# Optimization experiments

Measured on AMD Instinct MI355X. Metric: run time of the kernel, lower is better.

The kernel has to match this reference:

```python
import jax, jax.numpy as jnp
import numpy as np

B, L_R, H = 8, 128, 512
CTX_LEN, STATE_NUM, ACT_NUM = 256, 32, 32
L_SRC = CTX_LEN + STATE_NUM + ACT_NUM
N_VOCAB = 32000
N_TOPIC = 4096


def setup_inputs() -> dict:
    key = jax.random.key(0)
    ks = jax.random.split(key, 9)
    return {
        "dec_out": jax.random.normal(ks[0], (B, L_R, H), jnp.float32),
        "src_hidden": jax.random.normal(ks[1], (B, L_SRC, H), jnp.float32),
        "W_gen": jax.random.normal(ks[2], (H, N_VOCAB), jnp.float32) * 0.02,
        "b_gen": jnp.zeros((N_VOCAB,), jnp.float32),
        "src_mask": jax.random.randint(ks[3], (B, 1, L_SRC), 0, 2, jnp.int32),
        "context": jax.random.randint(ks[4], (B, CTX_LEN), 0, N_VOCAB, jnp.int32),
        "tp": jax.random.randint(ks[5], (B, STATE_NUM), 0, N_TOPIC, jnp.int32),
        "action": jax.random.randint(ks[6], (B, ACT_NUM), 0, N_TOPIC, jnp.int32),
        "loc2glo": jax.random.randint(ks[7], (N_TOPIC,), 0, N_VOCAB, jnp.int32),
    }


def _scatter_vocab(prob, idx):
    # prob: [L_r, L_seg], idx: [L_seg] global-vocab ids -> [L_r, n_vocab]
    # duplicate indices accumulate, matching torch scatter_add / one-hot bmm
    return jnp.zeros((prob.shape[0], N_VOCAB), prob.dtype).at[:, idx].add(prob)


def reference(dec_out, src_hidden, W_gen, b_gen, src_mask, context, tp, action, loc2glo):
    # gen logits: [B, L_r, n_vocab]
    gen_logit = jnp.einsum("blh,hv->blv", dec_out, W_gen) + b_gen
    # copy logits over concatenated source: [B, L_r, L_src]
    copy_logit = jnp.einsum("blh,bsh->bls", dec_out, src_hidden)
    copy_logit = jnp.where(src_mask == 0, jnp.float32(-1e9), copy_logit)
    logits = jnp.concatenate([gen_logit, copy_logit], axis=-1)
    logits = logits * (H ** -0.5)  # op.scale_prj
    probs = jax.nn.softmax(logits, axis=-1)

    gen_prob = probs[:, :, :N_VOCAB]
    copy_ctx = probs[:, :, N_VOCAB:N_VOCAB + CTX_LEN]
    copy_tp = probs[:, :, N_VOCAB + CTX_LEN:N_VOCAB + CTX_LEN + STATE_NUM]
    copy_ar = probs[:, :, N_VOCAB + CTX_LEN + STATE_NUM:]

    scatter = jax.vmap(_scatter_vocab)
    ctx_prob = scatter(copy_ctx, context)                 # replaces one-hot bmm
    tp_prob = scatter(copy_tp, loc2glo[tp])               # scatter_add via loc2glo gather
    ar_prob = scatter(copy_ar, loc2glo[action])

    return gen_prob + ctx_prob + tp_prob + ar_prob
```

## Files before the change

kernel.cpp:

```cpp
#include <hip/hip_runtime.h>
#include <stdint.h>
#include <stddef.h>

#define NV    32000
#define HDIM  512
#define LSRC  320
#define MROWS 1024
#define SCALEF 0.044194173824159216f

typedef unsigned short u16;
typedef unsigned int   u32;
typedef __attribute__((ext_vector_type(8))) short short8;
typedef __attribute__((ext_vector_type(4))) float floatx4;

__device__ __forceinline__ u16 f2bf(float f) {
  u32 x = __float_as_uint(f);
  return (u16)((x + 0x7fffu + ((x >> 16) & 1u)) >> 16);
}

typedef __attribute__((address_space(1))) void gvoid;
typedef __attribute__((address_space(3))) void lvoid;
__device__ __forceinline__ void cp16(const u16* g, u16* l) {
  __builtin_amdgcn_global_load_lds((gvoid*)g, (lvoid*)l, 16, 0, 0);
}

__global__ __launch_bounds__(256) void k_conv(const float* __restrict__ dec,
                                              const float* __restrict__ srch,
                                              u16* __restrict__ Ab,
                                              u16* __restrict__ Sb,
                                              float* __restrict__ rowSum) {
  if (blockIdx.x < 256) {
    if (blockIdx.x == 0) {
      ((float4*)rowSum)[threadIdx.x] = (float4){0.f, 0.f, 0.f, 0.f};
    }
    int t = blockIdx.x * 256 + threadIdx.x;
    int o = t * 8;
    int ki = o & 31;
    int mi = (o >> 5) & 255;
    int kt = (o >> 13) & 15;
    int mt = o >> 17;
    const float* s = dec + (size_t)(mt * 256 + mi) * HDIM + kt * 32 + ki;
    float4 a = ((const float4*)s)[0];
    float4 b = ((const float4*)s)[1];
    union { u16 h[8]; uint4 v; } pk;
    pk.h[0] = f2bf(a.x); pk.h[1] = f2bf(a.y); pk.h[2] = f2bf(a.z); pk.h[3] = f2bf(a.w);
    pk.h[4] = f2bf(b.x); pk.h[5] = f2bf(b.y); pk.h[6] = f2bf(b.z); pk.h[7] = f2bf(b.w);
    *(uint4*)(Ab + o) = pk.v;
  } else {
    int t = (blockIdx.x - 256) * 256 + threadIdx.x;
    int o = t * 8;
    int ki = o & 31;
    int ni = (o >> 5) & 127;
    int kt = (o >> 12) & 15;
    int r  = o >> 16;
    int st = r % 3, b = r / 3;
    int s = st * 128 + ni;
    uint4 v;
    if (s < LSRC) {
      const float* p = srch + ((size_t)b * LSRC + s) * HDIM + kt * 32 + ki;
      float4 a = ((const float4*)p)[0];
      float4 c = ((const float4*)p)[1];
      union { u16 h[8]; uint4 u; } pk;
      pk.h[0] = f2bf(a.x); pk.h[1] = f2bf(a.y); pk.h[2] = f2bf(a.z); pk.h[3] = f2bf(a.w);
      pk.h[4] = f2bf(c.x); pk.h[5] = f2bf(c.y); pk.h[6] = f2bf(c.z); pk.h[7] = f2bf(c.w);
      v = pk.u;
    } else {
      v = (uint4){0u, 0u, 0u, 0u};
    }
    *(uint4*)(Sb + o) = v;
  }
}

__global__ __launch_bounds__(256) void k_convW(const float* __restrict__ W,
                                               u16* __restrict__ Wb) {
  __shared__ u16 lds[256 * 36];
  int tileId = blockIdx.x;
  int nt = tileId >> 4, kt = tileId & 15;
  int t = threadIdx.x;
  const float* src = W + (size_t)kt * 32 * NV + (size_t)nt * 256;
#pragma unroll
  for (int i = 0; i < 8; ++i) {
    int f = t + 256 * i;
    int kin = f >> 6, n4 = f & 63;
    float4 v = *(const float4*)(src + (size_t)kin * NV + n4 * 4);
    int base = (n4 * 4) * 36 + kin;
    lds[base]       = f2bf(v.x);
    lds[base + 36]  = f2bf(v.y);
    lds[base + 72]  = f2bf(v.z);
    lds[base + 108] = f2bf(v.w);
  }
  __syncthreads();
  u16* dst = Wb + (size_t)tileId * 8192;
#pragma unroll
  for (int j = 0; j < 4; ++j) {
    int o = t * 8 + j * 2048;
    int ni = o >> 5, ki0 = o & 31;
    const u16* p = &lds[ni * 36 + ki0];
    uint2 x = *(const uint2*)p;
    uint2 y = *(const uint2*)(p + 4);
    uint4 v; v.x = x.x; v.y = x.y; v.z = y.x; v.w = y.y;
    *(uint4*)(dst + o) = v;
  }
}

__global__ __launch_bounds__(512, 2) void k_gemm(const u16* __restrict__ Ab,
                                                 const u16* __restrict__ Wb,
                                                 const float* __restrict__ bgen,
                                                 u16* __restrict__ wsE,
                                                 float* __restrict__ rowSum) {
  __shared__ u16 As[3][8192];
  __shared__ u16 Bs[3][8192];
  int bid = blockIdx.x;
  int xcd = bid & 7, rem = bid >> 3;
  int wgid = (xcd < 4 ? xcd * 63 : 252 + (xcd - 4) * 62) + rem;
  int x = wgid & 3, y = wgid >> 2;
  int t = threadIdx.x;
  int wid = t >> 6, lane = t & 63;
  int wm = wid >> 2, wn = wid & 3;
  int quad = lane >> 4, l16 = lane & 15;

  const u16* At = Ab + (size_t)x * (16 * 8192);
  const u16* Bt = Wb + (size_t)y * (16 * 8192);
  const u16* Ag0 = At + wid * 512 + lane * 8;
  const u16* Bg0 = Bt + wid * 512 + lane * 8;

  floatx4 acc[8][4];
#pragma unroll
  for (int i = 0; i < 8; ++i)
#pragma unroll
    for (int j = 0; j < 4; ++j) acc[i][j] = (floatx4){0.f, 0.f, 0.f, 0.f};

#pragma unroll
  for (int p = 0; p < 2; ++p) {
    const u16* ag = Ag0 + p * 8192;
    const u16* bg = Bg0 + p * 8192;
    cp16(ag,        &As[p][wid * 512]);
    cp16(ag + 4096, &As[p][wid * 512 + 4096]);
    cp16(bg,        &Bs[p][wid * 512]);
    cp16(bg + 4096, &Bs[p][wid * 512 + 4096]);
  }

#pragma unroll
  for (int kt = 0; kt < 16; ++kt) {
    const int cb = kt % 3;
    asm volatile("s_waitcnt lgkmcnt(0)" ::: "memory");
    if (kt < 15) asm volatile("s_waitcnt vmcnt(4)" ::: "memory");
    else         asm volatile("s_waitcnt vmcnt(0)" ::: "memory");
    __builtin_amdgcn_s_barrier();
    asm volatile("" ::: "memory");
    if (kt < 14) {
      const int sb = (kt + 2) % 3;
      const u16* ag = Ag0 + (kt + 2) * 8192;
      const u16* bg = Bg0 + (kt + 2) * 8192;
      cp16(ag,        &As[sb][wid * 512]);
      cp16(ag + 4096, &As[sb][wid * 512 + 4096]);
      cp16(bg,        &Bs[sb][wid * 512]);
      cp16(bg + 4096, &Bs[sb][wid * 512 + 4096]);
    }
    short8 aR[8], bR[4];
#pragma unroll
    for (int mt = 0; mt < 8; ++mt)
      aR[mt] = *(const short8*)&As[cb][(wm * 128 + mt * 16 + l16) * 32 + quad * 8];
#pragma unroll
    for (int nt = 0; nt < 4; ++nt)
      bR[nt] = *(const short8*)&Bs[cb][(wn * 64 + nt * 16 + l16) * 32 + quad * 8];
    __builtin_amdgcn_s_setprio(1);
#pragma unroll
    for (int mt = 0; mt < 8; ++mt)
#pragma unroll
      for (int nt = 0; nt < 4; ++nt)
        acc[mt][nt] = __builtin_amdgcn_mfma_f32_16x16x32_bf16(bR[nt], aR[mt],
                                                              acc[mt][nt], 0, 0, 0);
    __builtin_amdgcn_s_setprio(0);
  }

  int row0 = x * 256 + wm * 128;
  int col0 = y * 256 + wn * 64;
  float bq[4][4];
#pragma unroll
  for (int nt = 0; nt < 4; ++nt) {
    float4 v = *(const float4*)(bgen + col0 + nt * 16 + quad * 4);
    bq[nt][0] = v.x * SCALEF; bq[nt][1] = v.y * SCALEF;
    bq[nt][2] = v.z * SCALEF; bq[nt][3] = v.w * SCALEF;
  }
#pragma unroll
  for (int mt = 0; mt < 8; ++mt) {
    int row = row0 + mt * 16 + l16;
    float rsum = 0.f;
#pragma unroll
    for (int nt = 0; nt < 4; ++nt) {
      float e0 = __expf(fmaf(acc[mt][nt][0], SCALEF, bq[nt][0]));
      float e1 = __expf(fmaf(acc[mt][nt][1], SCALEF, bq[nt][1]));
      float e2 = __expf(fmaf(acc[mt][nt][2], SCALEF, bq[nt][2]));
      float e3 = __expf(fmaf(acc[mt][nt][3], SCALEF, bq[nt][3]));
      uint2 pk;
      pk.x = (u32)f2bf(e0) | ((u32)f2bf(e1) << 16);
      pk.y = (u32)f2bf(e2) | ((u32)f2bf(e3) << 16);
      *(uint2*)(wsE + (size_t)row * NV + col0 + nt * 16 + quad * 4) = pk;
      rsum += (e0 + e1) + (e2 + e3);
    }
    rsum += __shfl_xor(rsum, 16, 64);
    rsum += __shfl_xor(rsum, 32, 64);
    if (lane < 16) atomicAdd(&rowSum[row], rsum);
  }
}

__global__ __launch_bounds__(256) void k_copy(const u16* __restrict__ Ab,
                                              const u16* __restrict__ Sb,
                                              const int* __restrict__ mask,
                                              float* __restrict__ wsCopy,
                                              float* __restrict__ rowSum) {
  __shared__ u16 As[3][4096];
  __shared__ u16 Bs[3][4096];
  int bid = blockIdx.x;
  int b = bid / 3, st = bid % 3;
  int t = threadIdx.x;
  int wid = t >> 6, lane = t & 63;
  int wm = wid >> 1, wn = wid & 1;
  int quad = lane >> 4, l16 = lane & 15;

  const u16* At = Ab + (size_t)(b >> 1) * (16 * 8192) + (b & 1) * 4096;
  const u16* Bt = Sb + (size_t)(b * 3 + st) * (16 * 4096);
  const u16* Ag0 = At + wid * 1024 + lane * 8;
  const u16* Bg0 = Bt + wid * 1024 + lane * 8;

  floatx4 acc[4][4];
#pragma unroll
  for (int i = 0; i < 4; ++i)
#pragma unroll
    for (int j = 0; j < 4; ++j) acc[i][j] = (floatx4){0.f, 0.f, 0.f, 0.f};

#pragma unroll
  for (int p = 0; p < 2; ++p) {
    const u16* ag = Ag0 + p * 8192;
    const u16* bg = Bg0 + p * 4096;
    cp16(ag,       &As[p][wid * 1024]);
    cp16(ag + 512, &As[p][wid * 1024 + 512]);
    cp16(bg,       &Bs[p][wid * 1024]);
    cp16(bg + 512, &Bs[p][wid * 1024 + 512]);
  }

#pragma unroll
  for (int kt = 0; kt < 16; ++kt) {
    const int cb = kt % 3;
    asm volatile("s_waitcnt lgkmcnt(0)" ::: "memory");
    if (kt < 15) asm volatile("s_waitcnt vmcnt(4)" ::: "memory");
    else         asm volatile("s_waitcnt vmcnt(0)" ::: "memory");
    __builtin_amdgcn_s_barrier();
    asm volatile("" ::: "memory");
    if (kt < 14) {
      const int sb = (kt + 2) % 3;
      const u16* ag = Ag0 + (kt + 2) * 8192;
      const u16* bg = Bg0 + (kt + 2) * 4096;
      cp16(ag,       &As[sb][wid * 1024]);
      cp16(ag + 512, &As[sb][wid * 1024 + 512]);
      cp16(bg,       &Bs[sb][wid * 1024]);
      cp16(bg + 512, &Bs[sb][wid * 1024 + 512]);
    }
    short8 aR[4], bR[4];
#pragma unroll
    for (int mt = 0; mt < 4; ++mt)
      aR[mt] = *(const short8*)&As[cb][(wm * 64 + mt * 16 + l16) * 32 + quad * 8];
#pragma unroll
    for (int nt = 0; nt < 4; ++nt)
      bR[nt] = *(const short8*)&Bs[cb][(wn * 64 + nt * 16 + l16) * 32 + quad * 8];
#pragma unroll
    for (int mt = 0; mt < 4; ++mt)
#pragma unroll
      for (int nt = 0; nt < 4; ++nt)
        acc[mt][nt] = __builtin_amdgcn_mfma_f32_16x16x32_bf16(bR[nt], aR[mt],
                                                              acc[mt][nt], 0, 0, 0);
  }

  int row0 = b * 128 + wm * 64;
  int sBase = st * 128 + wn * 64;
  if (sBase < LSRC) {
    int mq[4][4];
#pragma unroll
    for (int nt = 0; nt < 4; ++nt) {
      int4 v = *(const int4*)(mask + b * LSRC + sBase + nt * 16 + quad * 4);
      mq[nt][0] = v.x; mq[nt][1] = v.y; mq[nt][2] = v.z; mq[nt][3] = v.w;
    }
#pragma unroll
    for (int mt = 0; mt < 4; ++mt) {
      int row = row0 + mt * 16 + l16;
      float rsum = 0.f;
#pragma unroll
      for (int nt = 0; nt < 4; ++nt) {
        float4 ev;
        ev.x = mq[nt][0] ? __expf(acc[mt][nt][0] * SCALEF) : 0.f;
        ev.y = mq[nt][1] ? __expf(acc[mt][nt][1] * SCALEF) : 0.f;
        ev.z = mq[nt][2] ? __expf(acc[mt][nt][2] * SCALEF) : 0.f;
        ev.w = mq[nt][3] ? __expf(acc[mt][nt][3] * SCALEF) : 0.f;
        *(float4*)(wsCopy + (size_t)row * LSRC + sBase + nt * 16 + quad * 4) = ev;
        rsum += (ev.x + ev.y) + (ev.z + ev.w);
      }
      rsum += __shfl_xor(rsum, 16, 64);
      rsum += __shfl_xor(rsum, 32, 64);
      if (lane < 16) atomicAdd(&rowSum[row], rsum);
    }
  }
}

__global__ __launch_bounds__(512) void k_norm(const u16* __restrict__ wsE,
                                              const float* __restrict__ wsCopy,
                                              const float* __restrict__ rowSum,
                                              const int* __restrict__ context,
                                              const int* __restrict__ tp,
                                              const int* __restrict__ action,
                                              const int* __restrict__ loc2glo,
                                              float* __restrict__ out) {
  int r = blockIdx.x, b = r >> 7;
  float inv = 1.0f / rowSum[r];
  const uint2* src = (const uint2*)(wsE + (size_t)r * NV);
  float4* dst = (float4*)(out + (size_t)r * NV);
  for (int c = threadIdx.x; c < NV / 4; c += 512) {
    uint2 v = src[c];
    float4 o;
    o.x = __uint_as_float(v.x << 16) * inv;
    o.y = __uint_as_float(v.x & 0xffff0000u) * inv;
    o.z = __uint_as_float(v.y << 16) * inv;
    o.w = __uint_as_float(v.y & 0xffff0000u) * inv;
    dst[c] = o;
  }
  __syncthreads();
  int t = threadIdx.x;
  float* op = out + (size_t)r * NV;
  if (t < 256) {
    atomicAdd(op + context[b * 256 + t], wsCopy[r * LSRC + t] * inv);
  } else if (t < 288) {
    int i = t - 256;
    atomicAdd(op + loc2glo[tp[b * 32 + i]], wsCopy[r * LSRC + 256 + i] * inv);
  } else if (t < 320) {
    int i = t - 288;
    atomicAdd(op + loc2glo[action[b * 32 + i]], wsCopy[r * LSRC + 288 + i] * inv);
  }
}

extern "C" void kernel_launch(void* const* d_in, const int* in_sizes, int n_in,
                              void* d_out, int out_size, void* d_ws, size_t ws_size,
                              hipStream_t stream) {
  const float* dec  = (const float*)d_in[0];
  const float* srch = (const float*)d_in[1];
  const float* Wg   = (const float*)d_in[2];
  const float* bg   = (const float*)d_in[3];
  const int*   mask = (const int*)d_in[4];
  const int*   ctx  = (const int*)d_in[5];
  const int*   tp   = (const int*)d_in[6];
  const int*   act  = (const int*)d_in[7];
  const int*   l2g  = (const int*)d_in[8];
  float* out = (float*)d_out;

  char* ws = (char*)d_ws;
  u16*   Wb      = (u16*)(ws);
  u16*   wsE     = (u16*)(ws + 32768000);
  u16*   Ab      = (u16*)(ws + 98304000);
  float* wsCopy  = (float*)(ws + 99352576);
  float* rowSum  = (float*)(ws + 100663296);
  u16*   Sb      = (u16*)(ws + 100667392);

  hipLaunchKernelGGL(k_conv, dim3(1024), dim3(256), 0, stream, dec, srch, Ab, Sb, rowSum);
  hipLaunchKernelGGL(k_convW, dim3(2000), dim3(256), 0, stream, Wg, Wb);
  hipLaunchKernelGGL(k_gemm, dim3(500), dim3(512), 0, stream, Ab, Wb, bg, wsE, rowSum);
  hipLaunchKernelGGL(k_copy, dim3(24), dim3(256), 0, stream, Ab, Sb, mask, wsCopy, rowSum);
  hipLaunchKernelGGL(k_norm, dim3(MROWS), dim3(512), 0, stream, wsE, wsCopy, rowSum,
                     ctx, tp, act, l2g, out);
}
```

Before: 324.8 us.

## Fold copy-logit GEMM into main GEMM grid and deepen LDS pipeline

Removes the separate k_copy launch. The copy logits now run as 12 extra 256x256 tiles in the main GEMM grid (512 blocks, a clean 64 per XCD), with the source hidden states repacked into 256-wide tiles that pair two batches. The GEMM main loop goes from 3 to 4 LDS stages and splits each k-step into two half-MFMA phases with staggered async loads and extra barriers, aiming for better load/compute overlap. The copy tiles waste some compute on cross-batch products that are masked off, and the larger LDS footprint (128 KB per block) may limit occupancy.

```diff
diff --git a/kernel.cpp b/kernel.cpp
--- a/kernel.cpp
+++ b/kernel.cpp
@@ -23,6 +23,7 @@
 __device__ __forceinline__ void cp16(const u16* g, u16* l) {
   __builtin_amdgcn_global_load_lds((gvoid*)g, (lvoid*)l, 16, 0, 0);
 }
+#define BARRIER() do { __builtin_amdgcn_s_barrier(); asm volatile("" ::: "memory"); } while (0)
 
 __global__ __launch_bounds__(256) void k_conv(const float* __restrict__ dec,
                                               const float* __restrict__ srch,
@@ -50,19 +51,23 @@
     int t = (blockIdx.x - 256) * 256 + threadIdx.x;
     int o = t * 8;
     int ki = o & 31;
-    int ni = (o >> 5) & 127;
-    int kt = (o >> 12) & 15;
-    int r  = o >> 16;
-    int st = r % 3, b = r / 3;
-    int s = st * 128 + ni;
+    int ni = (o >> 5) & 255;
+    int kt = (o >> 13) & 15;
+    int r  = o >> 17;
+    int yt = r % 3, x = r / 3;
+    int c = yt * 256 + ni;
+    int b, s, valid;
+    if (c < 320)      { b = x * 2;     s = c;       valid = 1; }
+    else if (c < 640) { b = x * 2 + 1; s = c - 320; valid = 1; }
+    else              { b = 0; s = 0; valid = 0; }
     uint4 v;
-    if (s < LSRC) {
+    if (valid) {
       const float* p = srch + ((size_t)b * LSRC + s) * HDIM + kt * 32 + ki;
       float4 a = ((const float4*)p)[0];
-      float4 c = ((const float4*)p)[1];
+      float4 cc = ((const float4*)p)[1];
       union { u16 h[8]; uint4 u; } pk;
-      pk.h[0] = f2bf(a.x); pk.h[1] = f2bf(a.y); pk.h[2] = f2bf(a.z); pk.h[3] = f2bf(a.w);
-      pk.h[4] = f2bf(c.x); pk.h[5] = f2bf(c.y); pk.h[6] = f2bf(c.z); pk.h[7] = f2bf(c.w);
+      pk.h[0] = f2bf(a.x);  pk.h[1] = f2bf(a.y);  pk.h[2] = f2bf(a.z);  pk.h[3] = f2bf(a.w);
+      pk.h[4] = f2bf(cc.x); pk.h[5] = f2bf(cc.y); pk.h[6] = f2bf(cc.z); pk.h[7] = f2bf(cc.w);
       v = pk.u;
     } else {
       v = (uint4){0u, 0u, 0u, 0u};
@@ -105,14 +110,17 @@
 
 __global__ __launch_bounds__(512, 2) void k_gemm(const u16* __restrict__ Ab,
                                                  const u16* __restrict__ Wb,
+                                                 const u16* __restrict__ Sb,
                                                  const float* __restrict__ bgen,
+                                                 const int* __restrict__ mask,
                                                  u16* __restrict__ wsE,
+                                                 float* __restrict__ wsCopy,
                                                  float* __restrict__ rowSum) {
-  __shared__ u16 As[3][8192];
-  __shared__ u16 Bs[3][8192];
+  __shared__ u16 As[4][8192];
+  __shared__ u16 Bs[4][8192];
   int bid = blockIdx.x;
-  int xcd = bid & 7, rem = bid >> 3;
-  int wgid = (xcd < 4 ? xcd * 63 : 252 + (xcd - 4) * 62) + rem;
+  int xcd = bid & 7;
+  int wgid = xcd * 64 + (bid >> 3);
   int x = wgid & 3, y = wgid >> 2;
   int t = threadIdx.x;
   int wid = t >> 6, lane = t & 63;
@@ -120,7 +128,8 @@
   int quad = lane >> 4, l16 = lane & 15;
 
   const u16* At = Ab + (size_t)x * (16 * 8192);
-  const u16* Bt = Wb + (size_t)y * (16 * 8192);
+  const u16* Bt = (y < 125) ? (Wb + (size_t)y * (16 * 8192))
+                            : (Sb + (size_t)(x * 3 + (y - 125)) * (16 * 8192));
   const u16* Ag0 = At + wid * 512 + lane * 8;
   const u16* Bg0 = Bt + wid * 512 + lane * 8;
 
@@ -131,7 +140,7 @@
     for (int j = 0; j < 4; ++j) acc[i][j] = (floatx4){0.f, 0.f, 0.f, 0.f};
 
 #pragma unroll
-  for (int p = 0; p < 2; ++p) {
+  for (int p = 0; p < 3; ++p) {
     const u16* ag = Ag0 + p * 8192;
     const u16* bg = Bg0 + p * 8192;
     cp16(ag,        &As[p][wid * 512]);
@@ -139,150 +148,108 @@
     cp16(bg,        &Bs[p][wid * 512]);
     cp16(bg + 4096, &Bs[p][wid * 512 + 4096]);
   }
-
-#pragma unroll
-  for (int kt = 0; kt < 16; ++kt) {
-    const int cb = kt % 3;
+  asm volatile("s_waitcnt vmcnt(8)" ::: "memory");
+  BARRIER();
+
+#pragma unroll
+  for (int h = 0; h < 16; ++h) {
+    const int slot = h & 3;
+    const int ps = (h + 3) & 3;
+    const u16* ag = Ag0 + (h + 3) * 8192;
+    const u16* bg = Bg0 + (h + 3) * 8192;
+    short8 aR[4], bR[4];
+#pragma unroll
+    for (int mt = 0; mt < 4; ++mt)
+      aR[mt] = *(const short8*)&As[slot][(wm * 128 + mt * 16 + l16) * 32 + quad * 8];
+#pragma unroll
+    for (int nt = 0; nt < 4; ++nt)
+      bR[nt] = *(const short8*)&Bs[slot][(wn * 64 + nt * 16 + l16) * 32 + quad * 8];
+    if (h < 13) {
+      cp16(ag, &As[ps][wid * 512]);
+      cp16(bg, &Bs[ps][wid * 512]);
+    }
+    BARRIER();
     asm volatile("s_waitcnt lgkmcnt(0)" ::: "memory");
-    if (kt < 15) asm volatile("s_waitcnt vmcnt(4)" ::: "memory");
-    else         asm volatile("s_waitcnt vmcnt(0)" ::: "memory");
-    __builtin_amdgcn_s_barrier();
-    asm volatile("" ::: "memory");
-    if (kt < 14) {
-      const int sb = (kt + 2) % 3;
-      const u16* ag = Ag0 + (kt + 2) * 8192;
-      const u16* bg = Bg0 + (kt + 2) * 8192;
-      cp16(ag,        &As[sb][wid * 512]);
-      cp16(ag + 4096, &As[sb][wid * 512 + 4096]);
-      cp16(bg,        &Bs[sb][wid * 512]);
-      cp16(bg + 4096, &Bs[sb][wid * 512 + 4096]);
-    }
-    short8 aR[8], bR[4];
-#pragma unroll
-    for (int mt = 0; mt < 8; ++mt)
-      aR[mt] = *(const short8*)&As[cb][(wm * 128 + mt * 16 + l16) * 32 + quad * 8];
-#pragma unroll
-    for (int nt = 0; nt < 4; ++nt)
-      bR[nt] = *(const short8*)&Bs[cb][(wn * 64 + nt * 16 + l16) * 32 + quad * 8];
     __builtin_amdgcn_s_setprio(1);
 #pragma unroll
-    for (int mt = 0; mt < 8; ++mt)
+    for (int mt = 0; mt < 4; ++mt)
 #pragma unroll
       for (int nt = 0; nt < 4; ++nt)
         acc[mt][nt] = __builtin_amdgcn_mfma_f32_16x16x32_bf16(bR[nt], aR[mt],
                                                               acc[mt][nt], 0, 0, 0);
     __builtin_amdgcn_s_setprio(0);
+    BARRIER();
+#pragma unroll
+    for (int mt = 0; mt < 4; ++mt)
+      aR[mt] = *(const short8*)&As[slot][(wm * 128 + (mt + 4) * 16 + l16) * 32 + quad * 8];
+    if (h < 13) {
+      cp16(ag + 4096, &As[ps][wid * 512 + 4096]);
+      cp16(bg + 4096, &Bs[ps][wid * 512 + 4096]);
+    }
+    if (h < 13)      asm volatile("s_waitcnt vmcnt(8)" ::: "memory");
+    else if (h == 13) asm volatile("s_waitcnt vmcnt(4)" ::: "memory");
+    else             asm volatile("s_waitcnt vmcnt(0)" ::: "memory");
+    BARRIER();
+    asm volatile("s_waitcnt lgkmcnt(0)" ::: "memory");
+    __builtin_amdgcn_s_setprio(1);
+#pragma unroll
+    for (int mt = 0; mt < 4; ++mt)
+#pragma unroll
+      for (int nt = 0; nt < 4; ++nt)
+        acc[mt + 4][nt] = __builtin_amdgcn_mfma_f32_16x16x32_bf16(bR[nt], aR[mt],
+                                                                  acc[mt + 4][nt], 0, 0, 0);
+    __builtin_amdgcn_s_setprio(0);
+    BARRIER();
   }
 
   int row0 = x * 256 + wm * 128;
-  int col0 = y * 256 + wn * 64;
-  float bq[4][4];
-#pragma unroll
-  for (int nt = 0; nt < 4; ++nt) {
-    float4 v = *(const float4*)(bgen + col0 + nt * 16 + quad * 4);
-    bq[nt][0] = v.x * SCALEF; bq[nt][1] = v.y * SCALEF;
-    bq[nt][2] = v.z * SCALEF; bq[nt][3] = v.w * SCALEF;
-  }
-#pragma unroll
-  for (int mt = 0; mt < 8; ++mt) {
-    int row = row0 + mt * 16 + l16;
-    float rsum = 0.f;
+  if (y < 125) {
+    int col0 = y * 256 + wn * 64;
+    float bq[4][4];
 #pragma unroll
     for (int nt = 0; nt < 4; ++nt) {
-      float e0 = __expf(fmaf(acc[mt][nt][0], SCALEF, bq[nt][0]));
-      float e1 = __expf(fmaf(acc[mt][nt][1], SCALEF, bq[nt][1]));
-      float e2 = __expf(fmaf(acc[mt][nt][2], SCALEF, bq[nt][2]));
-      float e3 = __expf(fmaf(acc[mt][nt][3], SCALEF, bq[nt][3]));
-      uint2 pk;
-      pk.x = (u32)f2bf(e0) | ((u32)f2bf(e1) << 16);
-      pk.y = (u32)f2bf(e2) | ((u32)f2bf(e3) << 16);
-      *(uint2*)(wsE + (size_t)row * NV + col0 + nt * 16 + quad * 4) = pk;
-      rsum += (e0 + e1) + (e2 + e3);
-    }
-    rsum += __shfl_xor(rsum, 16, 64);
-    rsum += __shfl_xor(rsum, 32, 64);
-    if (lane < 16) atomicAdd(&rowSum[row], rsum);
-  }
-}
-
-__global__ __launch_bounds__(256) void k_copy(const u16* __restrict__ Ab,
-                                              const u16* __restrict__ Sb,
-                                              const int* __restrict__ mask,
-                                              float* __restrict__ wsCopy,
-                                              float* __restrict__ rowSum) {
-  __shared__ u16 As[3][4096];
-  __shared__ u16 Bs[3][4096];
-  int bid = blockIdx.x;
-  int b = bid / 3, st = bid % 3;
-  int t = threadIdx.x;
-  int wid = t >> 6, lane = t & 63;
-  int wm = wid >> 1, wn = wid & 1;
-  int quad = lane >> 4, l16 = lane & 15;
-
-  const u16* At = Ab + (size_t)(b >> 1) * (16 * 8192) + (b & 1) * 4096;
-  const u16* Bt = Sb + (size_t)(b * 3 + st) * (16 * 4096);
-  const u16* Ag0 = At + wid * 1024 + lane * 8;
-  const u16* Bg0 = Bt + wid * 1024 + lane * 8;
-
-  floatx4 acc[4][4];
-#pragma unroll
-  for (int i = 0; i < 4; ++i)
-#pragma unroll
-    for (int j = 0; j < 4; ++j) acc[i][j] = (floatx4){0.f, 0.f, 0.f, 0.f};
-
-#pragma unroll
-  for (int p = 0; p < 2; ++p) {
-    const u16* ag = Ag0 + p * 8192;
-    const u16* bg = Bg0 + p * 4096;
-    cp16(ag,       &As[p][wid * 1024]);
-    cp16(ag + 512, &As[p][wid * 1024 + 512]);
-    cp16(bg,       &Bs[p][wid * 1024]);
-    cp16(bg + 512, &Bs[p][wid * 1024 + 512]);
-  }
-
-#pragma unroll
-  for (int kt = 0; kt < 16; ++kt) {
-    const int cb = kt % 3;
-    asm volatile("s_waitcnt lgkmcnt(0)" ::: "memory");
-    if (kt < 15) asm volatile("s_waitcnt vmcnt(4)" ::: "memory");
-    else         asm volatile("s_waitcnt vmcnt(0)" ::: "memory");
-    __builtin_amdgcn_s_barrier();
-    asm volatile("" ::: "memory");
-    if (kt < 14) {
-      const int sb = (kt + 2) % 3;
-      const u16* ag = Ag0 + (kt + 2) * 8192;
-      const u16* bg = Bg0 + (kt + 2) * 4096;
-      cp16(ag,       &As[sb][wid * 1024]);
-      cp16(ag + 512, &As[sb][wid * 1024 + 512]);
-      cp16(bg,       &Bs[sb][wid * 1024]);
-      cp16(bg + 512, &Bs[sb][wid * 1024 + 512]);
-    }
-    short8 aR[4], bR[4];
-#pragma unroll
-    for (int mt = 0; mt < 4; ++mt)
-      aR[mt] = *(const short8*)&As[cb][(wm * 64 + mt * 16 + l16) * 32 + quad * 8];
-#pragma unroll
-    for (int nt = 0; nt < 4; ++nt)
-      bR[nt] = *(const short8*)&Bs[cb][(wn * 64 + nt * 16 + l16) * 32 + quad * 8];
-#pragma unroll
-    for (int mt = 0; mt < 4; ++mt)
-#pragma unroll
-      for (int nt = 0; nt < 4; ++nt)
-        acc[mt][nt] = __builtin_amdgcn_mfma_f32_16x16x32_bf16(bR[nt], aR[mt],
-                                                              acc[mt][nt], 0, 0, 0);
-  }
-
-  int row0 = b * 128 + wm * 64;
-  int sBase = st * 128 + wn * 64;
-  if (sBase < LSRC) {
-    int mq[4][4];
+      float4 v = *(const float4*)(bgen + col0 + nt * 16 + quad * 4);
+      bq[nt][0] = v.x * SCALEF; bq[nt][1] = v.y * SCALEF;
+      bq[nt][2] = v.z * SCALEF; bq[nt][3] = v.w * SCALEF;
+    }
+#pragma unroll
+    for (int mt = 0; mt < 8; ++mt) {
+      int row = row0 + mt * 16 + l16;
+      float rsum = 0.f;
+#pragma unroll
+      for (int nt = 0; nt < 4; ++nt) {
+        float e0 = __expf(fmaf(acc[mt][nt][0], SCALEF, bq[nt][0]));
+        float e1 = __expf(fmaf(acc[mt][nt][1], SCALEF, bq[nt][1]));
+        float e2 = __expf(fmaf(acc[mt][nt][2], SCALEF, bq[nt][2]));
+        float e3 = __expf(fmaf(acc[mt][nt][3], SCALEF, bq[nt][3]));
+        uint2 pk;
+        pk.x = (u32)f2bf(e0) | ((u32)f2bf(e1) << 16);
+        pk.y = (u32)f2bf(e2) | ((u32)f2bf(e3) << 16);
+        *(uint2*)(wsE + (size_t)row * NV + col0 + nt * 16 + quad * 4) = pk;
+        rsum += (e0 + e1) + (e2 + e3);
+      }
+      rsum += __shfl_xor(rsum, 16, 64);
+      rsum += __shfl_xor(rsum, 32, 64);
+      if (lane < 16) atomicAdd(&rowSum[row], rsum);
+    }
+  } else {
+    int b = x * 2 + wm;
+    int sOff = wm * 320;
+    int mq[4][4], vq[4], sc[4];
 #pragma unroll
     for (int nt = 0; nt < 4; ++nt) {
-      int4 v = *(const int4*)(mask + b * LSRC + sBase + nt * 16 + quad * 4);
-      mq[nt][0] = v.x; mq[nt][1] = v.y; mq[nt][2] = v.z; mq[nt][3] = v.w;
-    }
-#pragma unroll
-    for (int mt = 0; mt < 4; ++mt) {
+      int cc = (y - 125) * 256 + wn * 64 + nt * 16 + quad * 4;
+      vq[nt] = (cc >= sOff) && (cc < sOff + 320);
+      sc[nt] = cc - sOff;
+      if (vq[nt]) {
+        int4 v = *(const int4*)(mask + b * LSRC + sc[nt]);
+        mq[nt][0] = v.x; mq[nt][1] = v.y; mq[nt][2] = v.z; mq[nt][3] = v.w;
+      } else {
+        mq[nt][0] = mq[nt][1] = mq[nt][2] = mq[nt][3] = 0;
+      }
+    }
+#pragma unroll
+    for (int mt = 0; mt < 8; ++mt) {
       int row = row0 + mt * 16 + l16;
       float rsum = 0.f;
 #pragma unroll
@@ -292,7 +259,8 @@
         ev.y = mq[nt][1] ? __expf(acc[mt][nt][1] * SCALEF) : 0.f;
         ev.z = mq[nt][2] ? __expf(acc[mt][nt][2] * SCALEF) : 0.f;
         ev.w = mq[nt][3] ? __expf(acc[mt][nt][3] * SCALEF) : 0.f;
-        *(float4*)(wsCopy + (size_t)row * LSRC + sBase + nt * 16 + quad * 4) = ev;
+        if (vq[nt])
+          *(float4*)(wsCopy + (size_t)row * LSRC + sc[nt]) = ev;
         rsum += (ev.x + ev.y) + (ev.z + ev.w);
       }
       rsum += __shfl_xor(rsum, 16, 64);
@@ -361,8 +329,8 @@
 
   hipLaunchKernelGGL(k_conv, dim3(1024), dim3(256), 0, stream, dec, srch, Ab, Sb, rowSum);
   hipLaunchKernelGGL(k_convW, dim3(2000), dim3(256), 0, stream, Wg, Wb);
-  hipLaunchKernelGGL(k_gemm, dim3(500), dim3(512), 0, stream, Ab, Wb, bg, wsE, rowSum);
-  hipLaunchKernelGGL(k_copy, dim3(24), dim3(256), 0, stream, Ab, Sb, mask, wsCopy, rowSum);
+  hipLaunchKernelGGL(k_gemm, dim3(512), dim3(512), 0, stream, Ab, Wb, Sb, bg, mask,
+                     wsE, wsCopy, rowSum);
   hipLaunchKernelGGL(k_norm, dim3(MROWS), dim3(512), 0, stream, wsE, wsCopy, rowSum,
                      ctx, tp, act, l2g, out);
 }
```

Result: faster. 313.3 us (-3.6%).
